# Kernel optimization log

Measured on AMD Instinct MI355X. Metric: run time of the kernel, lower is better.

Reference implementation:

```python
import jax, jax.numpy as jnp
import numpy as np

WIDTH = 1024
NH = 16
HD = 64
MBS = 16
B = 4
L = 2048
BASE_LR = 1.0
EPS = 1e-6


def gelu_tanh(x):
    return jax.nn.gelu(x, approximate=True)


def gelu_bwd(x):
    t = jnp.tanh(0.79788456 * x * (1 + 0.044715 * x * x))
    return 0.5 * x * ((1 - t * t) * (0.79788456 + 0.1070322243 * x * x)) + 0.5 * (1 + t)


def ln_fwd(x, g, b):
    mu = x.mean(-1, keepdims=True)
    var = ((x - mu) ** 2).mean(-1, keepdims=True)
    return g * ((x - mu) * jax.lax.rsqrt(var + EPS)) + b


def ln_l2_bwd(x, tgt, g, b):
    # grad of 0.5*||LN(x)-tgt||^2 wrt x
    mu = x.mean(-1, keepdims=True)
    var = ((x - mu) ** 2).mean(-1, keepdims=True)
    std = jnp.sqrt(var + EPS)
    xh = (x - mu) / std
    gx = (g * xh + b - tgt) * g
    return (gx - gx.mean(-1, keepdims=True) - xh * (gx * xh).mean(-1, keepdims=True)) / std


def adapter_forward(hidden_states, Wq, Wk, Wv, Wo, Wg, lr_w, lr_b,
                    learnable_token_idx, norm_w, norm_b, W1, b1, W2, b2,
                    post_w, post_b):
    Bb, Ll, width = hidden_states.shape
    nh, hd = norm_w.shape
    mbs = learnable_token_idx.shape[0]
    nc = Ll // mbs  # L chosen divisible by mini_batch_size

    def split_heads(x):  # [B,L,width] -> [B,nh,nc,mbs,hd]
        return x.reshape(Bb, Ll, nh, hd).transpose(0, 2, 1, 3).reshape(Bb, nh, nc, mbs, hd)

    XQ = split_heads(hidden_states @ Wq.T)
    XK = split_heads(hidden_states @ Wk.T)
    XV = split_heads(hidden_states @ Wv.T)

    # eta: learnable per-token lr gate (get_eta)
    X = hidden_states.reshape(Bb, nc, mbs, width)
    lr = jnp.einsum('bnkc,hdc->bhnkd', X, lr_w) + lr_b.reshape(1, nh, 1, 1, 1)
    lr = jax.nn.sigmoid(lr).transpose(0, 1, 2, 4, 3)  # [B,nh,nc,1,mbs]
    lr_eta = BASE_LR * lr / hd
    token_idx = jnp.clip(1.0 / jnp.arange(1, mbs + 1, dtype=hidden_states.dtype)
                         + learnable_token_idx, 0.0, None)
    token_eta = token_idx.reshape(1, 1, 1, mbs, 1)
    eta = token_eta * lr_eta  # [B,nh,nc,mbs,mbs]

    tril = jnp.tril(jnp.ones((mbs, mbs), dtype=hidden_states.dtype))
    lnw = norm_w.reshape(nh, 1, hd)
    lnb = norm_b.reshape(nh, 1, hd)

    def step(carry, xs):
        W1s, b1s, W2s, b2s = carry  # [B,nh,hd,4hd], [B,nh,1,4hd], [B,nh,4hd,hd], [B,nh,1,hd]
        XQm, XKm, XVm, etam = xs    # [B,nh,mbs,hd] x3, [B,nh,mbs,mbs]
        X1 = XKm
        Z1 = X1 @ W1s + b1s
        X2 = gelu_tanh(Z1)
        Z2 = X2 @ W2s + b2s
        gZ2 = ln_l2_bwd(Z2, XVm - XKm, lnw, lnb)
        gZ1 = (gZ2 @ jnp.swapaxes(W2s, -1, -2)) * gelu_bwd(Z1)
        eta_tril = etam * tril
        Attn1 = tril * (XQm @ jnp.swapaxes(X1, -1, -2))
        b1_bar = b1s - eta_tril @ gZ1
        Z1_bar = XQm @ W1s - (etam * Attn1) @ gZ1 + b1_bar
        X2_bar = gelu_tanh(Z1_bar)
        Attn2 = tril * (X2_bar @ jnp.swapaxes(X2, -1, -2))
        b2_bar = b2s - eta_tril @ gZ2
        Z2_bar = X2_bar @ W2s - (etam * Attn2) @ gZ2 + b2_bar
        last = etam[:, :, -1, :, None]  # [B,nh,mbs,1]
        W1n = W1s - jnp.swapaxes(last * X1, -1, -2) @ gZ1
        b1n = b1s - (last * gZ1).sum(-2, keepdims=True)
        W2n = W2s - jnp.swapaxes(last * X2, -1, -2) @ gZ2
        b2n = b2s - (last * gZ2).sum(-2, keepdims=True)
        XQW = XQm + ln_fwd(Z2_bar, lnw, lnb)
        return (W1n, b1n, W2n, b2n), XQW

    carry0 = (jnp.broadcast_to(W1, (Bb,) + W1.shape),
              jnp.broadcast_to(b1, (Bb,) + b1.shape),
              jnp.broadcast_to(W2, (Bb,) + W2.shape),
              jnp.broadcast_to(b2, (Bb,) + b2.shape))
    xs = tuple(jnp.moveaxis(t, 2, 0) for t in (XQ, XK, XV, eta))
    _, XQW = jax.lax.scan(step, carry0, xs)  # [nc,B,nh,mbs,hd]
    out = XQW.transpose(1, 0, 3, 2, 4).reshape(Bb, Ll, width)

    # post_norm (LayerNorm eps=1e-6)
    out = ln_fwd(out, post_w, post_b)
    # gate
    out = gelu_tanh(hidden_states @ Wg.T) * out
    # o_proj
    return out @ Wo.T


def setup_inputs():
    key = jax.random.key(0)
    ks = jax.random.split(key, 10)
    n = lambda k, s: jax.random.normal(k, s, dtype=jnp.float32) * 0.02
    return {
        'hidden_states': jax.random.normal(ks[0], (B, L, WIDTH), dtype=jnp.float32),
        'Wq': n(ks[1], (WIDTH, WIDTH)),
        'Wk': n(ks[2], (WIDTH, WIDTH)),
        'Wv': n(ks[3], (WIDTH, WIDTH)),
        'Wo': n(ks[4], (WIDTH, WIDTH)),
        'Wg': n(ks[5], (WIDTH, WIDTH)),
        'lr_w': n(ks[6], (NH, 1, WIDTH)),
        'lr_b': jnp.zeros((NH, 1), jnp.float32),
        'learnable_token_idx': jnp.zeros((MBS,), jnp.float32),
        'norm_w': jnp.ones((NH, HD), jnp.float32),
        'norm_b': jnp.zeros((NH, HD), jnp.float32),
        'W1': n(ks[7], (NH, HD, 4 * HD)),
        'b1': jnp.zeros((NH, 1, 4 * HD), jnp.float32),
        'W2': n(ks[8], (NH, 4 * HD, HD)),
        'b2': jnp.zeros((NH, 1, HD), jnp.float32),
        'post_w': jnp.ones((WIDTH,), jnp.float32),
        'post_b': jnp.zeros((WIDTH,), jnp.float32),
    }


def reference(hidden_states, Wq, Wk, Wv, Wo, Wg, lr_w, lr_b, learnable_token_idx,
              norm_w, norm_b, W1, b1, W2, b2, post_w, post_b):
    return adapter_forward(hidden_states, Wq, Wk, Wv, Wo, Wg, lr_w, lr_b,
                           learnable_token_idx, norm_w, norm_b, W1, b1, W2, b2,
                           post_w, post_b)
```

## Files before the change

### kernel.cpp

```cpp
#include <hip/hip_runtime.h>

#define WIDTH 1024
#define MBSZ 16
#define LLL 2048
#define NCHUNK 128

typedef __attribute__((ext_vector_type(4))) float f32x4;
typedef __attribute__((ext_vector_type(2))) float f32x2;
typedef __attribute__((ext_vector_type(8))) short short8;
typedef __attribute__((ext_vector_type(2))) unsigned u32x2;
typedef __attribute__((ext_vector_type(4))) unsigned u32x4;

#define MFMA16(a, b, c) __builtin_amdgcn_mfma_f32_16x16x32_bf16((a), (b), (c), 0, 0, 0)

__device__ __forceinline__ short f2bf(float f) {
  unsigned u = __float_as_uint(f);
  u = (u + 0x7FFFu + ((u >> 16) & 1u)) >> 16;
  return (short)u;
}
__device__ __forceinline__ float bf2f(short s) {
  return __uint_as_float(((unsigned)(unsigned short)s) << 16);
}
__device__ __forceinline__ unsigned cvt_pk(float lo, float hi) {
  unsigned r;
  asm("v_cvt_pk_bf16_f32 %0, %1, %2" : "=v"(r) : "v"(lo), "v"(hi));
  return r;
}
__device__ __forceinline__ float fast_e2u(float x) {
  return __builtin_amdgcn_exp2f(x * (2.30220776f + 0.10294322f * x * x));
}
__device__ __forceinline__ float gelu_f(float x) {
  float e = fast_e2u(x);
  return x * (1.0f - __builtin_amdgcn_rcpf(e + 1.0f));
}
__device__ __forceinline__ float gelu_bwd_f(float x) {
  float e = fast_e2u(x);
  float r = __builtin_amdgcn_rcpf(e + 1.0f);
  return 2.0f * x * r * (1.0f - r) * (0.79788456f + 0.1070322243f * x * x) + (1.0f - r);
}
__device__ __forceinline__ int w2row(int d) { return d * 264 + (d >> 3) * 24; }

__global__ __launch_bounds__(256) void gemm_bt(const float* __restrict__ A,
                                               const float* __restrict__ W,
                                               float* __restrict__ C) {
  __shared__ __align__(16) short sA[64][40];
  __shared__ __align__(16) short sB[64][40];
  const int tid = threadIdx.x;
  const int m0 = blockIdx.x * 64, n0 = blockIdx.y * 64;
  const int srow = tid >> 2, sk = (tid & 3) * 8;
  const int wv = tid >> 6, ln = tid & 63;
  const int fr = ln & 15, kh = (ln >> 4) * 8;
  f32x4 acc[4];
#pragma unroll
  for (int s = 0; s < 4; ++s) acc[s] = (f32x4){0.f, 0.f, 0.f, 0.f};
  const float* ga = A + (long)(m0 + srow) * 1024 + sk;
  const float* gw = W + (long)(n0 + srow) * 1024 + sk;
  for (int k0 = 0; k0 < 1024; k0 += 32) {
    f32x4 a0 = *(const f32x4*)(ga + k0);
    f32x4 a1 = *(const f32x4*)(ga + k0 + 4);
    f32x4 w0 = *(const f32x4*)(gw + k0);
    f32x4 w1 = *(const f32x4*)(gw + k0 + 4);
    short8 pa, pw;
    pa[0] = f2bf(a0[0]); pa[1] = f2bf(a0[1]); pa[2] = f2bf(a0[2]); pa[3] = f2bf(a0[3]);
    pa[4] = f2bf(a1[0]); pa[5] = f2bf(a1[1]); pa[6] = f2bf(a1[2]); pa[7] = f2bf(a1[3]);
    pw[0] = f2bf(w0[0]); pw[1] = f2bf(w0[1]); pw[2] = f2bf(w0[2]); pw[3] = f2bf(w0[3]);
    pw[4] = f2bf(w1[0]); pw[5] = f2bf(w1[1]); pw[6] = f2bf(w1[2]); pw[7] = f2bf(w1[3]);
    *(short8*)&sA[srow][sk] = pa;
    *(short8*)&sB[srow][sk] = pw;
    __syncthreads();
    short8 af = *(const short8*)&sA[wv * 16 + fr][kh];
#pragma unroll
    for (int s = 0; s < 4; ++s) {
      short8 bf8 = *(const short8*)&sB[s * 16 + fr][kh];
      acc[s] = MFMA16(af, bf8, acc[s]);
    }
    __syncthreads();
  }
  const int orow = m0 + wv * 16 + (ln >> 4) * 4;
#pragma unroll
  for (int s = 0; s < 4; ++s)
#pragma unroll
    for (int q = 0; q < 4; ++q)
      C[(long)(orow + q) * 1024 + n0 + s * 16 + fr] = acc[s][q];
}

__global__ __launch_bounds__(256) void lr_kernel(const float* __restrict__ hs,
                                                 const float* __restrict__ lrw,
                                                 const float* __restrict__ lrb,
                                                 float* __restrict__ out) {
  __shared__ __align__(16) float row[1024];
  const int t = blockIdx.x, tid = threadIdx.x;
  *(f32x4*)&row[tid * 4] = *(const f32x4*)&hs[(long)t * 1024 + tid * 4];
  __syncthreads();
  const int hh = tid >> 4, j = tid & 15;
  const float* wrow = lrw + hh * 1024;
  float s = 0.f;
#pragma unroll 4
  for (int m = 0; m < 16; ++m) {
    const int c = j * 4 + m * 64;
    f32x4 x = *(const f32x4*)&row[c];
    f32x4 w = *(const f32x4*)&wrow[c];
    s += x[0] * w[0] + x[1] * w[1] + x[2] * w[2] + x[3] * w[3];
  }
#pragma unroll
  for (int o = 8; o; o >>= 1) s += __shfl_xor(s, o, 16);
  if (j == 0) {
    const float v = s + lrb[hh];
    const float sg = 1.f / (1.f + expf(-v));
    const int b = t >> 11, tr = t & 2047;
    out[((b << 4) + hh) * 2048 + tr] = sg * (1.f / 64.f);
  }
}

__global__ __launch_bounds__(512, 2) void scan_kernel(
    float* __restrict__ Qb, const float* __restrict__ Kb, const float* __restrict__ Vb,
    const float* __restrict__ LRb, const float* __restrict__ lti,
    const float* __restrict__ nw, const float* __restrict__ nb,
    const float* __restrict__ W1in, const float* __restrict__ b1in,
    const float* __restrict__ W2in, const float* __restrict__ b2in) {
  __shared__ __align__(16) short sW1b[256 * 72];
  __shared__ __align__(16) short sW2dp[64 * 264 + 192];
  __shared__ __align__(16) short la1T[64 * 24];
  __shared__ __align__(16) short la2T[256 * 24];
  __shared__ __align__(16) short sX1b[16 * 72];
  __shared__ __align__(16) short sXQb[16 * 72];
  __shared__ __align__(16) float sXQf[16 * 68];
  __shared__ __align__(16) float sTg[16 * 72];
  __shared__ __align__(16) short sX2b[16 * 264];
  __shared__ __align__(16) short sXbb[16 * 264];
  __shared__ __align__(16) short sG1c[256 * 24];
  __shared__ __align__(16) short sG2b[16 * 72];
  __shared__ __align__(16) short sG2c[64 * 24];
  __shared__ __align__(16) float sZ2f[16 * 68];
  __shared__ __align__(16) short sC1b[16 * 24];
  __shared__ __align__(16) short sC2b[16 * 24];
  __shared__ __align__(16) float sB1[256];
  __shared__ __align__(16) float sB2[64];
  __shared__ float sLr[16];
  __shared__ float sTok[16];
  __shared__ __align__(16) float sLnw[64];
  __shared__ __align__(16) float sLnb[64];

  const int bh = blockIdx.x, b = bh >> 4, h = bh & 15;
  const int tid = threadIdx.x;
  const int w = tid >> 6, ln = tid & 63;
  const int fr = ln & 15, half = ln >> 4, hk = half * 8;
  const int nt0 = 2 * w;

  float w1m[8][4], w2m[8][4];
#pragma unroll
  for (int r = 0; r < 8; ++r) {
    const int T = w * 8 + r, dt = T >> 4, pt = T & 15;
#pragma unroll
    for (int qq = 0; qq < 4; ++qq) {
      w1m[r][qq] = W1in[h * 16384 + (dt * 16 + half * 4 + qq) * 256 + pt * 16 + fr];
      w2m[r][qq] = W2in[h * 16384 + (pt * 16 + half * 4 + qq) * 64 + dt * 16 + fr];
    }
  }
  for (int e = tid; e < 16384; e += 512) {
    {
      const int d = e >> 8, p = e & 255;
      sW1b[p * 72 + d] = f2bf(W1in[h * 16384 + e]);
    }
    {
      const int p = e >> 6, d = e & 63;
      sW2dp[w2row(d) + (p ^ (((d >> 3) & 3) << 3))] = f2bf(W2in[h * 16384 + e]);
    }
  }
  if (tid < 256) sB1[tid] = b1in[h * 256 + tid];
  if (tid < 64) { sB2[tid] = b2in[h * 64 + tid]; sLnw[tid] = nw[h * 64 + tid]; sLnb[tid] = nb[h * 64 + tid]; }
  if (tid < 16) sTok[tid] = fmaxf(1.0f / (float)(tid + 1) + lti[tid], 0.0f);

  const f32x4 zf4 = (f32x4){0.f, 0.f, 0.f, 0.f};
  short8 zs8;
#pragma unroll
  for (int j = 0; j < 8; ++j) zs8[j] = 0;

  const int pf_i = tid >> 5;
  const int pf_d = (tid & 31) * 2;
  f32x2 pk, pq, pv;
  float plr = 0.f;
  {
    const long a0 = ((long)(b * LLL + pf_i)) * WIDTH + h * 64 + pf_d;
    pk = *(const f32x2*)&Kb[a0];
    pq = *(const f32x2*)&Qb[a0];
    pv = *(const f32x2*)&Vb[a0];
    if (tid < 16) plr = LRb[(long)bh * 2048 + tid];
  }

  for (int n = 0; n < NCHUNK; ++n) {
    const long gbase = ((long)(b * LLL + n * MBSZ)) * WIDTH + h * 64;

    {
      *(unsigned*)&sX1b[pf_i * 72 + pf_d] = cvt_pk(pk[0], pk[1]);
      *(unsigned*)&sXQb[pf_i * 72 + pf_d] = cvt_pk(pq[0], pq[1]);
      sXQf[pf_i * 68 + pf_d] = pq[0];
      sXQf[pf_i * 68 + pf_d + 1] = pq[1];
      sTg[pf_i * 72 + pf_d] = pv[0] - pk[0];
      sTg[pf_i * 72 + pf_d + 1] = pv[1] - pk[1];
      if (tid < 16) sLr[tid] = plr;
    }
    __syncthreads();

    short8 aX1[2], aXQ[2];
    aX1[0] = *(const short8*)&sX1b[fr * 72 + hk];
    aX1[1] = *(const short8*)&sX1b[fr * 72 + 32 + hk];
    aXQ[0] = *(const short8*)&sXQb[fr * 72 + hk];
    aXQ[1] = *(const short8*)&sXQb[fr * 72 + 32 + hk];
    f32x4 z1[2], q1[2];
    float b1p[2];
#pragma unroll
    for (int t = 0; t < 2; ++t) {
      const int p = (nt0 + t) * 16 + fr;
      z1[t] = zf4; q1[t] = zf4;
#pragma unroll
      for (int ks = 0; ks < 2; ++ks) {
        short8 bw = *(const short8*)&sW1b[p * 72 + ks * 32 + hk];
        z1[t] = MFMA16(aX1[ks], bw, z1[t]);
        q1[t] = MFMA16(aXQ[ks], bw, q1[t]);
      }
      b1p[t] = sB1[p];
#pragma unroll
      for (int qq = 0; qq < 4; ++qq) {
        z1[t][qq] += b1p[t];
        sX2b[(half * 4 + qq) * 264 + p] = f2bf(gelu_f(z1[t][qq]));
      }
    }
    {
      const float tok15 = sTok[15];
      const int d = tid >> 3, j0 = (tid & 7) * 2;
      const float v0 = bf2f(sX1b[j0 * 72 + d]) * (tok15 * sLr[j0]);
      const float v1 = bf2f(sX1b[(j0 + 1) * 72 + d]) * (tok15 * sLr[j0 + 1]);
      *(unsigned*)&la1T[d * 24 + j0] = cvt_pk(v0, v1);
    }
    if (w == 0) {
      f32x4 c = MFMA16(aXQ[0], aX1[0], zf4);
      c = MFMA16(aXQ[1], aX1[1], c);
#pragma unroll
      for (int qq = 0; qq < 4; ++qq) {
        const int i = half * 4 + qq, j = fr;
        sC1b[i * 24 + j] = f2bf((i >= j) ? sTok[i] * sLr[j] * (c[qq] + 1.0f) : 0.0f);
      }
    }
    __syncthreads();

    float bb2old = 0.f;
    if (w < 4) {
      const int d = w * 16 + fr;
      const int sw = ((d >> 3) & 3) << 3;
      const int rb = w2row(d);
      f32x4 za = zf4, zb = zf4;
#pragma unroll
      for (int ks = 0; ks < 4; ++ks) {
        short8 a = *(const short8*)&sX2b[fr * 264 + ks * 32 + hk];
        short8 bfr = *(const short8*)&sW2dp[rb + ((ks * 32 + hk) ^ sw)];
        za = MFMA16(a, bfr, za);
      }
#pragma unroll
      for (int ks = 4; ks < 8; ++ks) {
        short8 a = *(const short8*)&sX2b[fr * 264 + ks * 32 + hk];
        short8 bfr = *(const short8*)&sW2dp[rb + ((ks * 32 + hk) ^ sw)];
        zb = MFMA16(a, bfr, zb);
      }
      bb2old = sB2[d];
#pragma unroll
      for (int qq = 0; qq < 4; ++qq)
        sZ2f[(half * 4 + qq) * 68 + d] = za[qq] + zb[qq] + bb2old;
    }
    __syncthreads();

    if (tid < 256) {
      const int i = tid >> 4, j4 = tid & 15;
      const f32x4 z = *(const f32x4*)&sZ2f[i * 68 + j4 * 4];
      float s1 = z[0] + z[1] + z[2] + z[3];
      float s2 = z[0] * z[0] + z[1] * z[1] + z[2] * z[2] + z[3] * z[3];
#pragma unroll
      for (int o = 8; o; o >>= 1) { s1 += __shfl_xor(s1, o, 16); s2 += __shfl_xor(s2, o, 16); }
      const float mu = s1 * (1.f / 64.f);
      const float rstd = rsqrtf(s2 * (1.f / 64.f) - mu * mu + 1e-6f);
      const f32x4 g = *(const f32x4*)&sLnw[j4 * 4];
      const f32x4 bb = *(const f32x4*)&sLnb[j4 * 4];
      const f32x4 tg = *(const f32x4*)&sTg[i * 72 + j4 * 4];
      f32x4 xh, gx;
      float a1 = 0.f, a2 = 0.f;
#pragma unroll
      for (int e = 0; e < 4; ++e) {
        xh[e] = (z[e] - mu) * rstd;
        gx[e] = (g[e] * xh[e] + bb[e] - tg[e]) * g[e];
        a1 += gx[e]; a2 += gx[e] * xh[e];
      }
#pragma unroll
      for (int o = 8; o; o >>= 1) { a1 += __shfl_xor(a1, o, 16); a2 += __shfl_xor(a2, o, 16); }
      const float m1 = a1 * (1.f / 64.f), m2 = a2 * (1.f / 64.f);
      float o4[4];
#pragma unroll
      for (int e = 0; e < 4; ++e) o4[e] = (gx[e] - m1 - xh[e] * m2) * rstd;
      const unsigned lo = cvt_pk(o4[0], o4[1]);
      const unsigned hi = cvt_pk(o4[2], o4[3]);
      *(u32x2*)&sG2b[i * 72 + j4 * 4] = (u32x2){lo, hi};
      sG2c[(j4 * 4 + 0) * 24 + i] = (short)lo;
      sG2c[(j4 * 4 + 1) * 24 + i] = (short)(lo >> 16);
      sG2c[(j4 * 4 + 2) * 24 + i] = (short)hi;
      sG2c[(j4 * 4 + 3) * 24 + i] = (short)(hi >> 16);
    } else {
      const int pp = tid - 256;
      const float tok15 = sTok[15];
      unsigned uu[8];
#pragma unroll
      for (int jp = 0; jp < 8; ++jp) {
        const float v0 = bf2f(sX2b[(2 * jp) * 264 + pp]) * (tok15 * sLr[2 * jp]);
        const float v1 = bf2f(sX2b[(2 * jp + 1) * 264 + pp]) * (tok15 * sLr[2 * jp + 1]);
        uu[jp] = cvt_pk(v0, v1);
      }
      *(u32x4*)&la2T[pp * 24] = (u32x4){uu[0], uu[1], uu[2], uu[3]};
      *(u32x4*)&la2T[pp * 24 + 8] = (u32x4){uu[4], uu[5], uu[6], uu[7]};
    }
    __syncthreads();

    {
      short8 aG2[2];
      aG2[0] = *(const short8*)&sG2b[fr * 72 + hk];
      aG2[1] = *(const short8*)&sG2b[fr * 72 + 32 + hk];
#pragma unroll
      for (int t = 0; t < 2; ++t) {
        const int p = (nt0 + t) * 16 + fr;
        f32x4 g = zf4;
#pragma unroll
        for (int ks = 0; ks < 2; ++ks) {
          const int dg = ks * 32 + hk;
          const int rb = w2row(dg) + (p ^ (((dg >> 3) & 3) << 3));
          short8 bw;
#pragma unroll
          for (int jj = 0; jj < 8; ++jj) bw[jj] = sW2dp[rb + jj * 264];
          g = MFMA16(aG2[ks], bw, g);
        }
        const unsigned lo = cvt_pk(g[0] * gelu_bwd_f(z1[t][0]), g[1] * gelu_bwd_f(z1[t][1]));
        const unsigned hi = cvt_pk(g[2] * gelu_bwd_f(z1[t][2]), g[3] * gelu_bwd_f(z1[t][3]));
        *(u32x2*)&sG1c[p * 24 + half * 4] = (u32x2){lo, hi};
      }
    }
    if (tid < 64) {
      float s = 0.f;
#pragma unroll
      for (int j = 0; j < 16; ++j) s += sLr[j] * bf2f(sG2c[tid * 24 + j]);
      sB2[tid] -= sTok[15] * s;
    }
    __syncthreads();

    {
      short8 ac = zs8;
      if (half < 2) ac = *(const short8*)&sC1b[fr * 24 + hk];
#pragma unroll
      for (int t = 0; t < 2; ++t) {
        const int p = (nt0 + t) * 16 + fr;
        short8 bg = zs8;
        if (half < 2) bg = *(const short8*)&sG1c[p * 24 + hk];
        f32x4 corr = MFMA16(ac, bg, zf4);
#pragma unroll
        for (int qq = 0; qq < 4; ++qq)
          sXbb[(half * 4 + qq) * 264 + p] = f2bf(gelu_f(q1[t][qq] + b1p[t] - corr[qq]));
      }
    }
    {
#pragma unroll
      for (int r = 0; r < 8; ++r) {
        const int T = w * 8 + r, dt = T >> 4, pt = T & 15;
        short8 af = zs8, bg = zs8;
        if (half < 2) {
          af = *(const short8*)&la1T[(dt * 16 + fr) * 24 + hk];
          bg = *(const short8*)&sG1c[(pt * 16 + fr) * 24 + hk];
        }
        f32x4 dl = MFMA16(af, bg, zf4);
        const int pp = pt * 16 + fr, d0 = dt * 16 + half * 4;
        w1m[r][0] -= dl[0]; w1m[r][1] -= dl[1]; w1m[r][2] -= dl[2]; w1m[r][3] -= dl[3];
        const unsigned lo = cvt_pk(w1m[r][0], w1m[r][1]);
        const unsigned hi = cvt_pk(w1m[r][2], w1m[r][3]);
        *(u32x2*)&sW1b[pp * 72 + d0] = (u32x2){lo, hi};
      }
    }
    if (tid < 256) {
      float s = 0.f;
#pragma unroll
      for (int j = 0; j < 16; ++j) s += sLr[j] * bf2f(sG1c[tid * 24 + j]);
      sB1[tid] -= sTok[15] * s;
    }
    __syncthreads();

    {
      const int nn = (n + 1 < NCHUNK) ? n + 1 : n;
      const long a1 = ((long)(b * LLL + nn * MBSZ + pf_i)) * WIDTH + h * 64 + pf_d;
      pk = *(const f32x2*)&Kb[a1];
      pq = *(const f32x2*)&Qb[a1];
      pv = *(const f32x2*)&Vb[a1];
      if (tid < 16) plr = LRb[(long)bh * 2048 + nn * MBSZ + tid];
    }
    f32x4 zbar = zf4;
    if (w < 4) {
      const int d = w * 16 + fr;
      const int sw = ((d >> 3) & 3) << 3;
      const int rb = w2row(d);
      f32x4 za = zf4, zb = zf4;
#pragma unroll
      for (int ks = 0; ks < 4; ++ks) {
        short8 a = *(const short8*)&sXbb[fr * 264 + ks * 32 + hk];
        short8 bfr = *(const short8*)&sW2dp[rb + ((ks * 32 + hk) ^ sw)];
        za = MFMA16(a, bfr, za);
      }
#pragma unroll
      for (int ks = 4; ks < 8; ++ks) {
        short8 a = *(const short8*)&sXbb[fr * 264 + ks * 32 + hk];
        short8 bfr = *(const short8*)&sW2dp[rb + ((ks * 32 + hk) ^ sw)];
        zb = MFMA16(a, bfr, zb);
      }
      zbar[0] = za[0] + zb[0]; zbar[1] = za[1] + zb[1];
      zbar[2] = za[2] + zb[2]; zbar[3] = za[3] + zb[3];
    } else if (w == 4) {
      f32x4 c = zf4;
#pragma unroll
      for (int ks = 0; ks < 8; ++ks) {
        short8 a = *(const short8*)&sXbb[fr * 264 + ks * 32 + hk];
        short8 bx = *(const short8*)&sX2b[fr * 264 + ks * 32 + hk];
        c = MFMA16(a, bx, c);
      }
#pragma unroll
      for (int qq = 0; qq < 4; ++qq) {
        const int i = half * 4 + qq, j = fr;
        sC2b[i * 24 + j] = f2bf((i >= j) ? sTok[i] * sLr[j] * (c[qq] + 1.0f) : 0.0f);
      }
    }
    __syncthreads();

    if (w < 4) {
      const int d = w * 16 + fr;
      short8 ac = zs8, bg = zs8;
      if (half < 2) {
        ac = *(const short8*)&sC2b[fr * 24 + hk];
        bg = *(const short8*)&sG2c[d * 24 + hk];
      }
      f32x4 corr = MFMA16(ac, bg, zf4);
#pragma unroll
      for (int qq = 0; qq < 4; ++qq)
        sZ2f[(half * 4 + qq) * 68 + d] = zbar[qq] + bb2old - corr[qq];
    }
    {
#pragma unroll
      for (int r = 0; r < 8; ++r) {
        const int T = w * 8 + r, pt = T & 15, dt = T >> 4;
        short8 af = zs8, bg = zs8;
        if (half < 2) {
          af = *(const short8*)&la2T[(pt * 16 + fr) * 24 + hk];
          bg = *(const short8*)&sG2c[(dt * 16 + fr) * 24 + hk];
        }
        f32x4 dl = MFMA16(af, bg, zf4);
        const int dd = dt * 16 + fr;
        const int swp = ((dd >> 3) & 3) << 3;
        const int p0 = pt * 16 + half * 4;
        w2m[r][0] -= dl[0]; w2m[r][1] -= dl[1]; w2m[r][2] -= dl[2]; w2m[r][3] -= dl[3];
        const unsigned lo = cvt_pk(w2m[r][0], w2m[r][1]);
        const unsigned hi = cvt_pk(w2m[r][2], w2m[r][3]);
        *(u32x2*)&sW2dp[w2row(dd) + (p0 ^ swp)] = (u32x2){lo, hi};
      }
    }
    __syncthreads();

    if (tid < 256) {
      const int i = tid >> 4, j4 = tid & 15;
      const f32x4 z = *(const f32x4*)&sZ2f[i * 68 + j4 * 4];
      float s1 = z[0] + z[1] + z[2] + z[3];
      float s2 = z[0] * z[0] + z[1] * z[1] + z[2] * z[2] + z[3] * z[3];
#pragma unroll
      for (int o = 8; o; o >>= 1) { s1 += __shfl_xor(s1, o, 16); s2 += __shfl_xor(s2, o, 16); }
      const float mu = s1 * (1.f / 64.f);
      const float rstd = rsqrtf(s2 * (1.f / 64.f) - mu * mu + 1e-6f);
      const f32x4 g = *(const f32x4*)&sLnw[j4 * 4];
      const f32x4 bb = *(const f32x4*)&sLnb[j4 * 4];
      const f32x4 xq = *(const f32x4*)&sXQf[i * 68 + j4 * 4];
      f32x4 o4;
#pragma unroll
      for (int e = 0; e < 4; ++e) o4[e] = xq[e] + g[e] * ((z[e] - mu) * rstd) + bb[e];
      *(f32x4*)&Qb[gbase + (long)i * WIDTH + j4 * 4] = o4;
    }
    __syncthreads();
  }
}

__global__ __launch_bounds__(256) void epi_kernel(const float* __restrict__ X,
                                                  const float* __restrict__ G,
                                                  const float* __restrict__ pw,
                                                  const float* __restrict__ pb,
                                                  float* __restrict__ T) {
  __shared__ float red[8];
  const int t = blockIdx.x, tid = threadIdx.x;
  const long base = (long)t * 1024 + tid * 4;
  f32x4 x = *(const f32x4*)&X[base];
  float s1 = x[0] + x[1] + x[2] + x[3];
  float s2 = x[0] * x[0] + x[1] * x[1] + x[2] * x[2] + x[3] * x[3];
#pragma unroll
  for (int o = 32; o; o >>= 1) { s1 += __shfl_xor(s1, o, 64); s2 += __shfl_xor(s2, o, 64); }
  const int wv = tid >> 6, ln = tid & 63;
  if (ln == 0) { red[wv] = s1; red[4 + wv] = s2; }
  __syncthreads();
  s1 = red[0] + red[1] + red[2] + red[3];
  s2 = red[4] + red[5] + red[6] + red[7];
  const float mu = s1 * (1.f / 1024.f);
  const float rstd = rsqrtf(s2 * (1.f / 1024.f) - mu * mu + 1e-6f);
  f32x4 g = *(const f32x4*)&G[base];
  f32x4 w = *(const f32x4*)&pw[tid * 4];
  f32x4 bb = *(const f32x4*)&pb[tid * 4];
  f32x4 o4;
#pragma unroll
  for (int e = 0; e < 4; ++e) {
    float y = w[e] * ((x[e] - mu) * rstd) + bb[e];
    o4[e] = gelu_f(g[e]) * y;
  }
  *(f32x4*)&T[base] = o4;
}

extern "C" void kernel_launch(void* const* d_in, const int* in_sizes, int n_in,
                              void* d_out, int out_size, void* d_ws, size_t ws_size,
                              hipStream_t stream) {
  const float* hs  = (const float*)d_in[0];
  const float* Wq  = (const float*)d_in[1];
  const float* Wk  = (const float*)d_in[2];
  const float* Wv  = (const float*)d_in[3];
  const float* Wo  = (const float*)d_in[4];
  const float* Wg  = (const float*)d_in[5];
  const float* lrw = (const float*)d_in[6];
  const float* lrb = (const float*)d_in[7];
  const float* lti = (const float*)d_in[8];
  const float* nw  = (const float*)d_in[9];
  const float* nb  = (const float*)d_in[10];
  const float* W1  = (const float*)d_in[11];
  const float* b1  = (const float*)d_in[12];
  const float* W2  = (const float*)d_in[13];
  const float* b2  = (const float*)d_in[14];
  const float* pw  = (const float*)d_in[15];
  const float* pb  = (const float*)d_in[16];
  float* out = (float*)d_out;
  float* ws = (float*)d_ws;

  float* Qb  = ws;
  float* Kb  = ws + 8388608;
  float* Vb  = ws + 16777216;
  float* Gb  = ws + 25165824;
  float* LRb = ws + 33554432;

  dim3 gg(128, 16);
  gemm_bt<<<gg, 256, 0, stream>>>(hs, Wq, Qb);
  gemm_bt<<<gg, 256, 0, stream>>>(hs, Wk, Kb);
  gemm_bt<<<gg, 256, 0, stream>>>(hs, Wv, Vb);
  gemm_bt<<<gg, 256, 0, stream>>>(hs, Wg, Gb);
  lr_kernel<<<8192, 256, 0, stream>>>(hs, lrw, lrb, LRb);
  scan_kernel<<<64, 512, 0, stream>>>(Qb, Kb, Vb, LRb, lti, nw, nb, W1, b1, W2, b2);
  epi_kernel<<<8192, 256, 0, stream>>>(Qb, Gb, pw, pb, Kb);
  gemm_bt<<<gg, 256, 0, stream>>>(Kb, Wo, out);
}
```

Measured before the change: 1.054 ms.

## Pre-convert GEMM operands to bf16 and store intermediates in bf16

Adds a single conversion kernel that turns hidden states and all five weight matrices into bf16 once, so the GEMMs load bf16 directly instead of loading fp32 and converting inside every tile. The gate projection now writes bf16 and runs after the scan. The epilogue reads the bf16 gate and writes its output in bf16 for the final GEMM. This halves GEMM operand traffic and removes repeated conversions, at the cost of an extra pass over about 13.6M elements and reduced precision in the gate and epilogue intermediates.

```diff
diff --git a/kernel.cpp b/kernel.cpp
--- a/kernel.cpp
+++ b/kernel.cpp
@@ -8,6 +8,7 @@
 typedef __attribute__((ext_vector_type(4))) float f32x4;
 typedef __attribute__((ext_vector_type(2))) float f32x2;
 typedef __attribute__((ext_vector_type(8))) short short8;
+typedef __attribute__((ext_vector_type(4))) short short4v;
 typedef __attribute__((ext_vector_type(2))) unsigned u32x2;
 typedef __attribute__((ext_vector_type(4))) unsigned u32x4;
 
@@ -40,9 +41,36 @@
 }
 __device__ __forceinline__ int w2row(int d) { return d * 264 + (d >> 3) * 24; }
 
-__global__ __launch_bounds__(256) void gemm_bt(const float* __restrict__ A,
-                                               const float* __restrict__ W,
-                                               float* __restrict__ C) {
+__global__ __launch_bounds__(256) void cvt_kernel(const float* __restrict__ hs,
+                                                  const float* __restrict__ Wq,
+                                                  const float* __restrict__ Wk,
+                                                  const float* __restrict__ Wv,
+                                                  const float* __restrict__ Wg,
+                                                  const float* __restrict__ Wo,
+                                                  short* __restrict__ dst) {
+  const long idx = ((long)blockIdx.x * 256 + threadIdx.x) * 8;
+  if (idx >= 13631488L) return;
+  const float* src;
+  long off;
+  if (idx < 8388608L)       { src = hs; off = idx; }
+  else if (idx < 9437184L)  { src = Wq; off = idx - 8388608L; }
+  else if (idx < 10485760L) { src = Wk; off = idx - 9437184L; }
+  else if (idx < 11534336L) { src = Wv; off = idx - 10485760L; }
+  else if (idx < 12582912L) { src = Wg; off = idx - 11534336L; }
+  else                      { src = Wo; off = idx - 12582912L; }
+  const f32x4 a = *(const f32x4*)(src + off);
+  const f32x4 b = *(const f32x4*)(src + off + 4);
+  u32x4 o;
+  o[0] = cvt_pk(a[0], a[1]); o[1] = cvt_pk(a[2], a[3]);
+  o[2] = cvt_pk(b[0], b[1]); o[3] = cvt_pk(b[2], b[3]);
+  *(u32x4*)(dst + idx) = o;
+}
+
+template <int OUTBF>
+__global__ __launch_bounds__(256) void gemm_bt_b(const short* __restrict__ A,
+                                                 const short* __restrict__ W,
+                                                 float* __restrict__ C,
+                                                 short* __restrict__ Cb) {
   __shared__ __align__(16) short sA[64][40];
   __shared__ __align__(16) short sB[64][40];
   const int tid = threadIdx.x;
@@ -53,20 +81,13 @@
   f32x4 acc[4];
 #pragma unroll
   for (int s = 0; s < 4; ++s) acc[s] = (f32x4){0.f, 0.f, 0.f, 0.f};
-  const float* ga = A + (long)(m0 + srow) * 1024 + sk;
-  const float* gw = W + (long)(n0 + srow) * 1024 + sk;
+  const short* ga = A + (long)(m0 + srow) * 1024 + sk;
+  const short* gw = W + (long)(n0 + srow) * 1024 + sk;
   for (int k0 = 0; k0 < 1024; k0 += 32) {
-    f32x4 a0 = *(const f32x4*)(ga + k0);
-    f32x4 a1 = *(const f32x4*)(ga + k0 + 4);
-    f32x4 w0 = *(const f32x4*)(gw + k0);
-    f32x4 w1 = *(const f32x4*)(gw + k0 + 4);
-    short8 pa, pw;
-    pa[0] = f2bf(a0[0]); pa[1] = f2bf(a0[1]); pa[2] = f2bf(a0[2]); pa[3] = f2bf(a0[3]);
-    pa[4] = f2bf(a1[0]); pa[5] = f2bf(a1[1]); pa[6] = f2bf(a1[2]); pa[7] = f2bf(a1[3]);
-    pw[0] = f2bf(w0[0]); pw[1] = f2bf(w0[1]); pw[2] = f2bf(w0[2]); pw[3] = f2bf(w0[3]);
-    pw[4] = f2bf(w1[0]); pw[5] = f2bf(w1[1]); pw[6] = f2bf(w1[2]); pw[7] = f2bf(w1[3]);
-    *(short8*)&sA[srow][sk] = pa;
-    *(short8*)&sB[srow][sk] = pw;
+    const short8 a8 = *(const short8*)(ga + k0);
+    const short8 w8 = *(const short8*)(gw + k0);
+    *(short8*)&sA[srow][sk] = a8;
+    *(short8*)&sB[srow][sk] = w8;
     __syncthreads();
     short8 af = *(const short8*)&sA[wv * 16 + fr][kh];
 #pragma unroll
@@ -80,8 +101,12 @@
 #pragma unroll
   for (int s = 0; s < 4; ++s)
 #pragma unroll
-    for (int q = 0; q < 4; ++q)
-      C[(long)(orow + q) * 1024 + n0 + s * 16 + fr] = acc[s][q];
+    for (int q = 0; q < 4; ++q) {
+      if (OUTBF)
+        Cb[(long)(orow + q) * 1024 + n0 + s * 16 + fr] = f2bf(acc[s][q]);
+      else
+        C[(long)(orow + q) * 1024 + n0 + s * 16 + fr] = acc[s][q];
+    }
 }
 
 __global__ __launch_bounds__(256) void lr_kernel(const float* __restrict__ hs,
@@ -485,10 +510,10 @@
 }
 
 __global__ __launch_bounds__(256) void epi_kernel(const float* __restrict__ X,
-                                                  const float* __restrict__ G,
+                                                  const short* __restrict__ G,
                                                   const float* __restrict__ pw,
                                                   const float* __restrict__ pb,
-                                                  float* __restrict__ T) {
+                                                  short* __restrict__ T) {
   __shared__ float red[8];
   const int t = blockIdx.x, tid = threadIdx.x;
   const long base = (long)t * 1024 + tid * 4;
@@ -504,16 +529,16 @@
   s2 = red[4] + red[5] + red[6] + red[7];
   const float mu = s1 * (1.f / 1024.f);
   const float rstd = rsqrtf(s2 * (1.f / 1024.f) - mu * mu + 1e-6f);
-  f32x4 g = *(const f32x4*)&G[base];
+  const short4v g4 = *(const short4v*)&G[base];
   f32x4 w = *(const f32x4*)&pw[tid * 4];
   f32x4 bb = *(const f32x4*)&pb[tid * 4];
-  f32x4 o4;
+  float o4[4];
 #pragma unroll
   for (int e = 0; e < 4; ++e) {
     float y = w[e] * ((x[e] - mu) * rstd) + bb[e];
-    o4[e] = gelu_f(g[e]) * y;
-  }
-  *(f32x4*)&T[base] = o4;
+    o4[e] = gelu_f(bf2f(g4[e])) * y;
+  }
+  *(u32x2*)&T[base] = (u32x2){cvt_pk(o4[0], o4[1]), cvt_pk(o4[2], o4[3])};
 }
 
 extern "C" void kernel_launch(void* const* d_in, const int* in_sizes, int n_in,
@@ -542,16 +567,24 @@
   float* Qb  = ws;
   float* Kb  = ws + 8388608;
   float* Vb  = ws + 16777216;
-  float* Gb  = ws + 25165824;
-  float* LRb = ws + 33554432;
+  float* LRb = ws + 25165824;
+  short* hsb = (short*)(ws + 25296896);
+  short* Wqb = hsb + 8388608;
+  short* Wkb = Wqb + 1048576;
+  short* Wvb = Wkb + 1048576;
+  short* Wgb = Wvb + 1048576;
+  short* Wob = Wgb + 1048576;
+  short* Tb  = (short*)Kb;
+  short* Gbb = (short*)Vb;
 
   dim3 gg(128, 16);
-  gemm_bt<<<gg, 256, 0, stream>>>(hs, Wq, Qb);
-  gemm_bt<<<gg, 256, 0, stream>>>(hs, Wk, Kb);
-  gemm_bt<<<gg, 256, 0, stream>>>(hs, Wv, Vb);
-  gemm_bt<<<gg, 256, 0, stream>>>(hs, Wg, Gb);
+  cvt_kernel<<<6656, 256, 0, stream>>>(hs, Wq, Wk, Wv, Wg, Wo, hsb);
+  gemm_bt_b<0><<<gg, 256, 0, stream>>>(hsb, Wqb, Qb, nullptr);
+  gemm_bt_b<0><<<gg, 256, 0, stream>>>(hsb, Wkb, Kb, nullptr);
+  gemm_bt_b<0><<<gg, 256, 0, stream>>>(hsb, Wvb, Vb, nullptr);
   lr_kernel<<<8192, 256, 0, stream>>>(hs, lrw, lrb, LRb);
   scan_kernel<<<64, 512, 0, stream>>>(Qb, Kb, Vb, LRb, lti, nw, nb, W1, b1, W2, b2);
-  epi_kernel<<<8192, 256, 0, stream>>>(Qb, Gb, pw, pb, Kb);
-  gemm_bt<<<gg, 256, 0, stream>>>(Kb, Wo, out);
-}
+  gemm_bt_b<1><<<gg, 256, 0, stream>>>(hsb, Wgb, nullptr, Gbb);
+  epi_kernel<<<8192, 256, 0, stream>>>(Qb, Gbb, pw, pb, Tb);
+  gemm_bt_b<0><<<gg, 256, 0, stream>>>(Tb, Wob, out, nullptr);
+}
```

Result: faster. 990.9 us (-6.0%).
